# Optimization experiments

Hardware: AMD Instinct MI355X
Metric: run time of the kernel (lower is better)

The kernel has to match this reference:

```python
import jax, jax.numpy as jnp
import numpy as np

N_EMBD = 384
N_HEAD = 6
HEAD_SIZE = N_EMBD // N_HEAD  # 64
B, T, S = 128, 256, 256
EPS = 1e-5


def setup_inputs() -> dict:
    key = jax.random.key(0)
    ks = jax.random.split(key, 20)
    w = lambda k, shape: (jax.random.normal(k, shape, dtype=jnp.float32) * 0.02)
    inp = {
        'x': jax.random.normal(ks[0], (B, T, N_EMBD), dtype=jnp.float32),
        'encoder_output': jax.random.normal(ks[1], (B, S, N_EMBD), dtype=jnp.float32),
        # masked self-attention heads (stacked over heads): [H, C, D]
        'wq1': w(ks[2], (N_HEAD, N_EMBD, HEAD_SIZE)),
        'wk1': w(ks[3], (N_HEAD, N_EMBD, HEAD_SIZE)),
        'wv1': w(ks[4], (N_HEAD, N_EMBD, HEAD_SIZE)),
        'proj1_w': w(ks[5], (N_EMBD, N_EMBD)),
        'proj1_b': jnp.zeros((N_EMBD,), jnp.float32),
        # cross-attention heads
        'wq2': w(ks[6], (N_HEAD, N_EMBD, HEAD_SIZE)),
        'wk2': w(ks[7], (N_HEAD, N_EMBD, HEAD_SIZE)),
        'wv2': w(ks[8], (N_HEAD, N_EMBD, HEAD_SIZE)),
        'proj2_w': w(ks[9], (N_EMBD, N_EMBD)),
        'proj2_b': jnp.zeros((N_EMBD,), jnp.float32),
        # feed-forward
        'ffn_w1': w(ks[10], (N_EMBD, 4 * N_EMBD)),
        'ffn_b1': jnp.zeros((4 * N_EMBD,), jnp.float32),
        'ffn_w2': w(ks[11], (4 * N_EMBD, N_EMBD)),
        'ffn_b2': jnp.zeros((N_EMBD,), jnp.float32),
        # layernorms
        'ln1_g': jnp.ones((N_EMBD,), jnp.float32), 'ln1_b': jnp.zeros((N_EMBD,), jnp.float32),
        'ln2_g': jnp.ones((N_EMBD,), jnp.float32), 'ln2_b': jnp.zeros((N_EMBD,), jnp.float32),
        'ln3_g': jnp.ones((N_EMBD,), jnp.float32), 'ln3_b': jnp.zeros((N_EMBD,), jnp.float32),
    }
    return inp


def _layernorm(x, g, b):
    mu = jnp.mean(x, axis=-1, keepdims=True)
    var = jnp.mean(jnp.square(x - mu), axis=-1, keepdims=True)
    return (x - mu) * jax.lax.rsqrt(var + EPS) * g + b


def _mha(xq, xkv, wq, wk, wv, proj_w, proj_b, causal):
    # NOTE: source scales by C**-0.5 with C = n_embd (not head_size)
    scale = jnp.asarray(N_EMBD, xq.dtype) ** -0.5
    q = jnp.einsum('btc,hcd->bhtd', xq, wq)
    k = jnp.einsum('bsc,hcd->bhsd', xkv, wk)
    v = jnp.einsum('bsc,hcd->bhsd', xkv, wv)
    wei = jnp.einsum('bhtd,bhsd->bhts', q, k) * scale
    if causal:
        Tq, Tk = xq.shape[1], xkv.shape[1]
        mask = jnp.tril(jnp.ones((Tq, Tk), dtype=bool))
        wei = jnp.where(mask, wei, jnp.asarray(-jnp.inf, wei.dtype))
    p = jax.nn.softmax(wei, axis=-1)  # dropout omitted (eval mode)
    o = jnp.einsum('bhts,bhsd->bhtd', p, v)
    Bq, H, Tq, D = o.shape
    o = o.transpose(0, 2, 1, 3).reshape(Bq, Tq, H * D)  # concat heads
    return o @ proj_w + proj_b


def reference(x, encoder_output,
              wq1, wk1, wv1, proj1_w, proj1_b,
              wq2, wk2, wv2, proj2_w, proj2_b,
              ffn_w1, ffn_b1, ffn_w2, ffn_b2,
              ln1_g, ln1_b, ln2_g, ln2_b, ln3_g, ln3_b):
    # x = x + masked self-attn(ln1(x))
    x = x + _mha(_layernorm(x, ln1_g, ln1_b), _layernorm(x, ln1_g, ln1_b),
                 wq1, wk1, wv1, proj1_w, proj1_b, causal=True)
    # x = x + cross-attn(ln2(x), encoder_output)  (no mask)
    x = x + _mha(_layernorm(x, ln2_g, ln2_b), encoder_output,
                 wq2, wk2, wv2, proj2_w, proj2_b, causal=False)
    # x = x + ffwd(ln3(x))
    h = _layernorm(x, ln3_g, ln3_b)
    x = x + (jax.nn.relu(h @ ffn_w1 + ffn_b1) @ ffn_w2 + ffn_b2)
    return x
```

## Files before the change

### kernel.cpp

```cpp
#include <hip/hip_runtime.h>
#include <hip/hip_bf16.h>

#define BB 128
#define TT 256
#define CC 384
#define HH 6
#define DD 64
#define NTOK 32768

typedef __attribute__((ext_vector_type(8))) short short8;
typedef __attribute__((ext_vector_type(4))) float f32x4;

__device__ __forceinline__ unsigned short f2bf(float f) {
  union { float f; unsigned int u; } v; v.f = f;
  unsigned int r = v.u + 0x7fff + ((v.u >> 16) & 1);
  return (unsigned short)(r >> 16);
}

__device__ __forceinline__ void glds16(const void* g, void* l) {
  __builtin_amdgcn_global_load_lds((const __attribute__((address_space(1))) void*)g,
                                   (__attribute__((address_space(3))) void*)l, 16, 0, 0);
}

__device__ __forceinline__ void vm_drain() {
  asm volatile("s_waitcnt vmcnt(0)" ::: "memory");
  __builtin_amdgcn_sched_barrier(0);
}

__global__ __launch_bounds__(256) void pack_t_k(
    const float* __restrict__ wq1, const float* __restrict__ wk1, const float* __restrict__ wv1,
    const float* __restrict__ wq2, const float* __restrict__ wk2, const float* __restrict__ wv2,
    const float* __restrict__ proj1_w, const float* __restrict__ proj2_w,
    const float* __restrict__ ffn_w1, const float* __restrict__ ffn_w2,
    unsigned short* __restrict__ W) {
  __shared__ unsigned short tile[64 * 72];
  const int id = blockIdx.x;
  const int tid = threadIdx.x;
  const float* src;
  unsigned short* dst;
  int ldIn, ldOut, i0, j0;
  if (id < 216) {
    int w = id / 36, rem = id - w * 36;
    int h = rem / 6, tr = rem - h * 6;
    const float* bases[6] = {wq1, wk1, wv1, wq2, wk2, wv2};
    const int dstOff[6] = {0, 147456, 294912, 442368, 589824, 737280};
    src = bases[w] + h * 24576;
    dst = W + dstOff[w] + h * 24576;
    ldIn = 64; ldOut = 384; i0 = tr * 64; j0 = 0;
  } else if (id < 288) {
    int t = id - 216;
    int which = t / 36; t -= which * 36;
    int tr = t / 6, tc = t - tr * 6;
    src = which ? proj2_w : proj1_w;
    dst = W + (which ? 1032192 : 884736);
    ldIn = 384; ldOut = 384; i0 = tr * 64; j0 = tc * 64;
  } else if (id < 432) {
    int t = id - 288;
    int tr = t / 24, tc = t - tr * 24;
    src = ffn_w1; dst = W + 1179648;
    ldIn = 1536; ldOut = 384; i0 = tr * 64; j0 = tc * 64;
  } else {
    int t = id - 432;
    int tr = t / 6, tc = t - tr * 6;
    src = ffn_w2; dst = W + 1769472;
    ldIn = 384; ldOut = 1536; i0 = tr * 64; j0 = tc * 64;
  }
#pragma unroll
  for (int p = 0; p < 4; ++p) {
    int chunk = p * 256 + tid;
    int r = chunk >> 4, c4 = chunk & 15;
    float4 f = *(const float4*)&src[(size_t)(i0 + r) * ldIn + j0 + c4 * 4];
    tile[(c4 * 4 + 0) * 72 + r] = f2bf(f.x);
    tile[(c4 * 4 + 1) * 72 + r] = f2bf(f.y);
    tile[(c4 * 4 + 2) * 72 + r] = f2bf(f.z);
    tile[(c4 * 4 + 3) * 72 + r] = f2bf(f.w);
  }
  __syncthreads();
#pragma unroll
  for (int p = 0; p < 2; ++p) {
    int chunk = p * 256 + tid;
    int j = chunk >> 3, i8 = chunk & 7;
    *(uint4*)&dst[(size_t)(j0 + j) * ldOut + i0 + i8 * 8] = *(const uint4*)&tile[j * 72 + i8 * 8];
  }
}

__global__ __launch_bounds__(256) void ln_k(const float* __restrict__ x,
                                            unsigned short* __restrict__ out,
                                            const float* __restrict__ gamma,
                                            const float* __restrict__ beta) {
  int row = blockIdx.x * 4 + (threadIdx.x >> 6);
  int lane = threadIdx.x & 63;
  const float2* xr = (const float2*)(x + (size_t)row * CC);
  float2 v[3];
  float s = 0.f;
#pragma unroll
  for (int j = 0; j < 3; ++j) { v[j] = xr[j * 64 + lane]; s += v[j].x + v[j].y; }
#pragma unroll
  for (int m = 1; m < 64; m <<= 1) s += __shfl_xor(s, m);
  float mu = s * (1.0f / CC);
  float vs = 0.f;
#pragma unroll
  for (int j = 0; j < 3; ++j) {
    float dx = v[j].x - mu, dy = v[j].y - mu;
    vs += dx * dx + dy * dy;
  }
#pragma unroll
  for (int m = 1; m < 64; m <<= 1) vs += __shfl_xor(vs, m);
  float rs = rsqrtf(vs * (1.0f / CC) + 1e-5f);
  unsigned int* orow = (unsigned int*)(out + (size_t)row * CC);
#pragma unroll
  for (int j = 0; j < 3; ++j) {
    int cidx = j * 64 + lane;
    float2 gmm = ((const float2*)gamma)[cidx];
    float2 bt = ((const float2*)beta)[cidx];
    unsigned int lo = f2bf((v[j].x - mu) * rs * gmm.x + bt.x);
    unsigned int hi = f2bf((v[j].y - mu) * rs * gmm.y + bt.y);
    orow[cidx] = lo | (hi << 16);
  }
}

template <int EPI, bool AF32, int BM>
__global__ __launch_bounds__(256) void gemm_k(const void* __restrict__ Ap, int lda,
                                              const unsigned short* __restrict__ Bt, int ldb,
                                              void* __restrict__ Cp, int ldc,
                                              const float* __restrict__ bias,
                                              int K, int nx) {
  constexpr int MI = BM / 32;
  constexpr int APASS = BM * 8 / 256;
  __shared__ unsigned short smem[BM * 64 + 8192];
  unsigned short* sA = smem;
  unsigned short* sB = smem + BM * 64;
  const int tid = threadIdx.x;
  const int chunkg = gridDim.x >> 3;
  const int wg = blockIdx.x;
  const int lg = (wg & 7) * chunkg + (wg >> 3);
  const int bx = lg % nx, by = lg / nx;
  const int m0 = by * BM;
  const int n0 = bx * 128;
  const int wid = tid >> 6, lane = tid & 63;
  const int wr = wid >> 1, wc = wid & 1;
  const int g = lane >> 4, c = lane & 15;

  f32x4 acc[MI][4] = {};
  float biasr[4];
  if (EPI >= 1) {
#pragma unroll
    for (int ni = 0; ni < 4; ++ni) biasr[ni] = bias[n0 + wc * 64 + ni * 16 + c];
  }

  const int nt = K >> 6;
  for (int t = 0; t < nt; ++t) {
    const int k0 = t * 64;
    if constexpr (!AF32) {
#pragma unroll
      for (int p = 0; p < APASS; ++p) {
        int chunk = p * 256 + tid;
        int row = chunk >> 3, grp = chunk & 7;
        const unsigned short* Ab = (const unsigned short*)Ap;
        glds16(&Ab[(size_t)(m0 + row) * lda + k0 + ((grp ^ (row & 7)) << 3)], &sA[chunk * 8]);
      }
    } else {
#pragma unroll
      for (int p = 0; p < APASS; ++p) {
        int chunk = p * 256 + tid;
        int row = chunk >> 3, grp = chunk & 7;
        int dst = row * 64 + ((grp ^ (row & 7)) << 3);
        const float* Af = (const float*)Ap + (size_t)(m0 + row) * lda + k0 + grp * 8;
        float4 f0 = *(const float4*)Af;
        float4 f1 = *(const float4*)(Af + 4);
        union { unsigned short h[8]; uint4 u; } t2;
        t2.h[0] = f2bf(f0.x); t2.h[1] = f2bf(f0.y); t2.h[2] = f2bf(f0.z); t2.h[3] = f2bf(f0.w);
        t2.h[4] = f2bf(f1.x); t2.h[5] = f2bf(f1.y); t2.h[6] = f2bf(f1.z); t2.h[7] = f2bf(f1.w);
        *(uint4*)&sA[dst] = t2.u;
      }
    }
#pragma unroll
    for (int p = 0; p < 4; ++p) {
      int chunk = p * 256 + tid;
      int row = chunk >> 3, grp = chunk & 7;
      glds16(&Bt[(size_t)(n0 + row) * ldb + k0 + ((grp ^ (row & 7)) << 3)], &sB[chunk * 8]);
    }
    vm_drain();
    __syncthreads();
#pragma unroll
    for (int kk = 0; kk < 2; ++kk) {
      short8 a[MI], b[4];
#pragma unroll
      for (int mi = 0; mi < MI; ++mi) {
        int r = wr * (BM / 2) + mi * 16 + c;
        a[mi] = *(const short8*)&sA[r * 64 + (((kk * 4 + g) ^ (r & 7)) << 3)];
      }
#pragma unroll
      for (int ni = 0; ni < 4; ++ni) {
        int rb = wc * 64 + ni * 16 + c;
        b[ni] = *(const short8*)&sB[rb * 64 + (((kk * 4 + g) ^ (rb & 7)) << 3)];
      }
#pragma unroll
      for (int mi = 0; mi < MI; ++mi)
#pragma unroll
        for (int ni = 0; ni < 4; ++ni)
          acc[mi][ni] = __builtin_amdgcn_mfma_f32_16x16x32_bf16(a[mi], b[ni], acc[mi][ni], 0, 0, 0);
    }
    __syncthreads();
  }

#pragma unroll
  for (int mi = 0; mi < MI; ++mi)
#pragma unroll
    for (int ni = 0; ni < 4; ++ni)
#pragma unroll
      for (int i = 0; i < 4; ++i) {
        int row = wr * (BM / 2) + mi * 16 + g * 4 + i;
        int col = wc * 64 + ni * 16 + c;
        float v = acc[mi][ni][i];
        if (EPI == 1) v = fmaxf(v + biasr[ni], 0.f);
        int gsw = (col >> 3) ^ ((row >> 2) & 7);
        smem[row * 128 + gsw * 8 + (col & 7)] = f2bf(v);
      }
  __syncthreads();
#pragma unroll
  for (int it = 0; it < BM / 16; ++it) {
    int chunk = it * 256 + tid;
    int row = chunk >> 4, c16 = chunk & 15;
    int gsw = c16 ^ ((row >> 2) & 7);
    *(uint4*)&((unsigned short*)Cp)[(size_t)(m0 + row) * ldc + n0 + c16 * 8] =
        *(const uint4*)&smem[row * 128 + gsw * 8];
  }
}

__global__ __launch_bounds__(256) void ffn2_k(const unsigned short* __restrict__ h1,
                                              const unsigned short* __restrict__ W2t,
                                              float* __restrict__ out,
                                              const float* __restrict__ b2,
                                              const float* __restrict__ res) {
  __shared__ unsigned short smem[26624];
  unsigned short* sA = smem;
  unsigned short* sB = smem + 2048;
  const int tid = threadIdx.x;
  const int wg = blockIdx.x;
  const int lg = (wg & 7) * (gridDim.x >> 3) + (wg >> 3);
  const int m0 = lg * 32;
  const int w = tid >> 6, lane = tid & 63;
  const int g = lane >> 4, c = lane & 15;

  f32x4 acc[2][6] = {};
  float biasr[6];
#pragma unroll
  for (int ni = 0; ni < 6; ++ni) biasr[ni] = b2[w * 96 + ni * 16 + c];

  for (int t = 0; t < 24; ++t) {
    const int k0 = t * 64;
    {
      int row = tid >> 3, grp = tid & 7;
      glds16(&h1[(size_t)(m0 + row) * 1536 + k0 + ((grp ^ (row & 7)) << 3)], &sA[tid * 8]);
    }
#pragma unroll
    for (int p = 0; p < 12; ++p) {
      int chunk = p * 256 + tid;
      int row = chunk >> 3, grp = chunk & 7;
      glds16(&W2t[(size_t)row * 1536 + k0 + ((grp ^ (row & 7)) << 3)], &sB[chunk * 8]);
    }
    vm_drain();
    __syncthreads();
#pragma unroll
    for (int kk = 0; kk < 2; ++kk) {
      short8 a[2], b[6];
#pragma unroll
      for (int mi = 0; mi < 2; ++mi) {
        int r = mi * 16 + c;
        a[mi] = *(const short8*)&sA[r * 64 + (((kk * 4 + g) ^ (r & 7)) << 3)];
      }
#pragma unroll
      for (int ni = 0; ni < 6; ++ni) {
        int rb = w * 96 + ni * 16 + c;
        b[ni] = *(const short8*)&sB[rb * 64 + (((kk * 4 + g) ^ (rb & 7)) << 3)];
      }
#pragma unroll
      for (int mi = 0; mi < 2; ++mi)
#pragma unroll
        for (int ni = 0; ni < 6; ++ni)
          acc[mi][ni] = __builtin_amdgcn_mfma_f32_16x16x32_bf16(a[mi], b[ni], acc[mi][ni], 0, 0, 0);
    }
    __syncthreads();
  }

  float* smf = (float*)smem;
#pragma unroll
  for (int mi = 0; mi < 2; ++mi)
#pragma unroll
    for (int ni = 0; ni < 6; ++ni)
#pragma unroll
      for (int i = 0; i < 4; ++i) {
        int row = mi * 16 + g * 4 + i;
        int col = w * 96 + ni * 16 + c;
        int gg = col >> 2;
        int sg = (gg & ~7) | ((gg ^ row) & 7);
        smf[row * 388 + sg * 4 + (col & 3)] = acc[mi][ni][i] + biasr[ni];
      }
  __syncthreads();
#pragma unroll
  for (int it = 0; it < 12; ++it) {
    int chunk = it * 256 + tid;
    int row = chunk / 96, gg = chunk % 96;
    int sg = (gg & ~7) | ((gg ^ row) & 7);
    float4 v = *(const float4*)&smf[row * 388 + sg * 4];
    float4 r = *(const float4*)&res[(size_t)(m0 + row) * 384 + gg * 4];
    float4 o;
    o.x = v.x + r.x; o.y = v.y + r.y; o.z = v.z + r.z; o.w = v.w + r.w;
    *(float4*)&out[(size_t)(m0 + row) * 384 + gg * 4] = o;
  }
}

__global__ __launch_bounds__(512, 2) void gemm_ln_k(
    const unsigned short* __restrict__ Ab, const unsigned short* __restrict__ Bt,
    const float* __restrict__ bias, const float* __restrict__ res,
    float* __restrict__ xc, const float* __restrict__ gamma,
    const float* __restrict__ beta, unsigned short* __restrict__ xn) {
  __shared__ unsigned short smem[28672];
  __shared__ float part[64][8];
  unsigned short* sA = smem;
  unsigned short* sB = smem + 4096;
  const int tid = threadIdx.x;
  const int chunkg = gridDim.x >> 3;
  const int wg = blockIdx.x;
  const int lg = (wg & 7) * chunkg + (wg >> 3);
  const int m0 = lg * 64;
  const int wid = tid >> 6, lane = tid & 63;
  const int wr = wid >> 2, wcg = wid & 3;
  const int g = lane >> 4, c = lane & 15;

  f32x4 acc[2][6] = {};
  float biasr[6], gam[6], bet[6];
#pragma unroll
  for (int ni = 0; ni < 6; ++ni) {
    int col = wcg * 96 + ni * 16 + c;
    biasr[ni] = bias[col]; gam[ni] = gamma[col]; bet[ni] = beta[col];
  }

  for (int t = 0; t < 6; ++t) {
    const int k0 = t * 64;
    {
      int chunk = tid;
      int row = chunk >> 3, grp = chunk & 7;
      glds16(&Ab[(size_t)(m0 + row) * 384 + k0 + ((grp ^ (row & 7)) << 3)], &sA[chunk * 8]);
    }
#pragma unroll
    for (int p = 0; p < 6; ++p) {
      int chunk = p * 512 + tid;
      int row = chunk >> 3, grp = chunk & 7;
      glds16(&Bt[(size_t)row * 384 + k0 + ((grp ^ (row & 7)) << 3)], &sB[chunk * 8]);
    }
    vm_drain();
    __syncthreads();
#pragma unroll
    for (int kk = 0; kk < 2; ++kk) {
      short8 a[2], b[6];
#pragma unroll
      for (int mi = 0; mi < 2; ++mi) {
        int r = wr * 32 + mi * 16 + c;
        a[mi] = *(const short8*)&sA[r * 64 + (((kk * 4 + g) ^ (r & 7)) << 3)];
      }
#pragma unroll
      for (int ni = 0; ni < 6; ++ni) {
        int rb = wcg * 96 + ni * 16 + c;
        b[ni] = *(const short8*)&sB[rb * 64 + (((kk * 4 + g) ^ (rb & 7)) << 3)];
      }
#pragma unroll
      for (int mi = 0; mi < 2; ++mi)
#pragma unroll
        for (int ni = 0; ni < 6; ++ni)
          acc[mi][ni] = __builtin_amdgcn_mfma_f32_16x16x32_bf16(a[mi], b[ni], acc[mi][ni], 0, 0, 0);
    }
    __syncthreads();
  }

#pragma unroll
  for (int mi = 0; mi < 2; ++mi)
#pragma unroll
    for (int i = 0; i < 4; ++i) {
      int row = m0 + wr * 32 + mi * 16 + g * 4 + i;
#pragma unroll
      for (int ni = 0; ni < 6; ++ni)
        acc[mi][ni][i] += biasr[ni] + res[(size_t)row * 384 + wcg * 96 + ni * 16 + c];
    }

#pragma unroll
  for (int mi = 0; mi < 2; ++mi)
#pragma unroll
    for (int i = 0; i < 4; ++i) {
      float s = 0.f, q = 0.f;
#pragma unroll
      for (int ni = 0; ni < 6; ++ni) { float v = acc[mi][ni][i]; s += v; q += v * v; }
#pragma unroll
      for (int m = 1; m < 16; m <<= 1) { s += __shfl_xor(s, m); q += __shfl_xor(q, m); }
      if (c == 0) {
        int lr = wr * 32 + mi * 16 + g * 4 + i;
        part[lr][wcg] = s;
        part[lr][4 + wcg] = q;
      }
    }
  __syncthreads();
  float mu[2][4], rs[2][4];
#pragma unroll
  for (int mi = 0; mi < 2; ++mi)
#pragma unroll
    for (int i = 0; i < 4; ++i) {
      int lr = wr * 32 + mi * 16 + g * 4 + i;
      float s = part[lr][0] + part[lr][1] + part[lr][2] + part[lr][3];
      float q = part[lr][4] + part[lr][5] + part[lr][6] + part[lr][7];
      float m_ = s * (1.0f / 384.f);
      mu[mi][i] = m_;
      rs[mi][i] = rsqrtf(q * (1.0f / 384.f) - m_ * m_ + 1e-5f);
    }

  float* bf = (float*)smem;
#pragma unroll
  for (int h = 0; h < 2; ++h) {
    __syncthreads();
    if (wr == h) {
#pragma unroll
      for (int mi = 0; mi < 2; ++mi)
#pragma unroll
        for (int ni = 0; ni < 6; ++ni)
#pragma unroll
          for (int i = 0; i < 4; ++i) {
            int lr = mi * 16 + g * 4 + i;
            bf[lr * 388 + wcg * 96 + ni * 16 + c] = acc[mi][ni][i];
          }
    }
    __syncthreads();
#pragma unroll
    for (int p = 0; p < 6; ++p) {
      int chunk = p * 512 + tid;
      int row = chunk / 96, gg = chunk % 96;
      float4 v = *(const float4*)&bf[row * 388 + gg * 4];
      *(float4*)&xc[(size_t)(m0 + h * 32 + row) * 384 + gg * 4] = v;
    }
  }

  __syncthreads();
#pragma unroll
  for (int mi = 0; mi < 2; ++mi)
#pragma unroll
    for (int ni = 0; ni < 6; ++ni)
#pragma unroll
      for (int i = 0; i < 4; ++i) {
        int lr = wr * 32 + mi * 16 + g * 4 + i;
        smem[lr * 392 + wcg * 96 + ni * 16 + c] =
            f2bf((acc[mi][ni][i] - mu[mi][i]) * rs[mi][i] * gam[ni] + bet[ni]);
      }
  __syncthreads();
#pragma unroll
  for (int p = 0; p < 6; ++p) {
    int chunk = p * 512 + tid;
    int row = chunk / 48, c8 = chunk % 48;
    *(uint4*)&xn[(size_t)(m0 + row) * 384 + c8 * 8] = *(const uint4*)&smem[row * 392 + c8 * 8];
  }
}

__device__ __forceinline__ int vt_off(int d, int sgrp) {
  return d * 256 + ((((sgrp + (d >> 3)) & 31) ^ (d & 7)) << 3);
}

template <bool CAUSAL>
__global__ __launch_bounds__(512, 2) void attn_k(const unsigned short* __restrict__ QKV,
                                                 unsigned short* __restrict__ O) {
  __shared__ unsigned short Ks[256 * 64];
  __shared__ unsigned short Vt[64 * 256];
  __shared__ unsigned short Ps[8][16 * 40];
  const int bh = blockIdx.x >> 1;
  const int half = blockIdx.x & 1;
  const int b = bh / HH, hh = bh - b * HH;
  const int tid = threadIdx.x, wid = tid >> 6, lane = tid & 63;
  const int g = lane >> 4, c = lane & 15;
  const unsigned short* base = QKV + (size_t)b * TT * 1152;

#pragma unroll
  for (int t = 0; t < 4; ++t) {
    int chunk = t * 512 + tid;
    int s = chunk >> 3, grp = chunk & 7;
    *(uint4*)&Ks[s * 64 + ((grp ^ (s & 7)) << 3)] =
        *(const uint4*)&base[(size_t)s * 1152 + 384 + hh * 64 + grp * 8];
    union { unsigned short h[8]; uint4 u; } tv;
    tv.u = *(const uint4*)&base[(size_t)s * 1152 + 768 + hh * 64 + grp * 8];
#pragma unroll
    for (int j = 0; j < 8; ++j) Vt[vt_off(grp * 8 + j, s >> 3) + (s & 7)] = tv.h[j];
  }
  __syncthreads();

  const float scale = 0.05103103630798287f;
  unsigned short* Pw = &Ps[wid][0];
  const int qr0 = half * 128 + wid * 16;

  short8 aq[2];
#pragma unroll
  for (int kk = 0; kk < 2; ++kk)
    aq[kk] = *(const short8*)&QKV[(size_t)(b * TT + qr0 + c) * 1152 + hh * 64 + kk * 32 + g * 8];

  f32x4 sacc[16] = {};
#pragma unroll
  for (int sj = 0; sj < 16; ++sj) {
    if (!CAUSAL || sj * 16 <= qr0) {
      int rk = sj * 16 + c;
      f32x4 z = sacc[sj];
      z = __builtin_amdgcn_mfma_f32_16x16x32_bf16(
          aq[0], *(const short8*)&Ks[rk * 64 + ((g ^ (rk & 7)) << 3)], z, 0, 0, 0);
      z = __builtin_amdgcn_mfma_f32_16x16x32_bf16(
          aq[1], *(const short8*)&Ks[rk * 64 + (((4 + g) ^ (rk & 7)) << 3)], z, 0, 0, 0);
      sacc[sj] = z;
    }
  }

  float inv[4];
#pragma unroll
  for (int i = 0; i < 4; ++i) {
    const int qr = qr0 + g * 4 + i;
    float mx = -1e30f;
#pragma unroll
    for (int sj = 0; sj < 16; ++sj) {
      if (!CAUSAL || sj * 16 <= qr0) {
        int s = sj * 16 + c;
        float v = sacc[sj][i] * scale;
        if (CAUSAL && s > qr) v = -1e30f;
        sacc[sj][i] = v;
        mx = fmaxf(mx, v);
      }
    }
#pragma unroll
    for (int m = 1; m < 16; m <<= 1) mx = fmaxf(mx, __shfl_xor(mx, m));
    float sum = 0.f;
#pragma unroll
    for (int sj = 0; sj < 16; ++sj) {
      if (!CAUSAL || sj * 16 <= qr0) {
        float p = __expf(sacc[sj][i] - mx);
        sacc[sj][i] = p;
        sum += p;
      }
    }
#pragma unroll
    for (int m = 1; m < 16; m <<= 1) sum += __shfl_xor(sum, m);
    inv[i] = 1.0f / sum;
  }

  f32x4 oacc[4] = {};
#pragma unroll
  for (int sk = 0; sk < 8; ++sk) {
    if (!CAUSAL || sk * 32 <= qr0) {
#pragma unroll
      for (int half_sj = 0; half_sj < 2; ++half_sj) {
        int sj = sk * 2 + half_sj;
#pragma unroll
        for (int i = 0; i < 4; ++i)
          Pw[(g * 4 + i) * 40 + half_sj * 16 + c] = f2bf(sacc[sj][i]);
      }
      short8 ap = *(const short8*)&Pw[c * 40 + g * 8];
#pragma unroll
      for (int dj = 0; dj < 4; ++dj) {
        short8 bv = *(const short8*)&Vt[vt_off(dj * 16 + c, sk * 4 + g)];
        oacc[dj] = __builtin_amdgcn_mfma_f32_16x16x32_bf16(ap, bv, oacc[dj], 0, 0, 0);
      }
    }
  }

  __syncthreads();
#pragma unroll
  for (int dj = 0; dj < 4; ++dj)
#pragma unroll
    for (int i = 0; i < 4; ++i) {
      int lr = wid * 16 + g * 4 + i;
      int col = dj * 16 + c;
      int gsw = (col >> 3) ^ ((lr >> 2) & 7);
      Ks[lr * 64 + gsw * 8 + (col & 7)] = f2bf(oacc[dj][i] * inv[i]);
    }
  __syncthreads();
#pragma unroll
  for (int it = 0; it < 2; ++it) {
    int chunk = it * 512 + tid;
    int row = chunk >> 3, c8 = chunk & 7;
    int gsw = c8 ^ ((row >> 2) & 7);
    *(uint4*)&O[(size_t)(b * TT + half * 128 + row) * CC + hh * 64 + c8 * 8] =
        *(const uint4*)&Ks[row * 64 + gsw * 8];
  }
}

extern "C" void kernel_launch(void* const* d_in, const int* in_sizes, int n_in,
                              void* d_out, int out_size, void* d_ws, size_t ws_size,
                              hipStream_t stream) {
  const float* x = (const float*)d_in[0];
  const float* enc = (const float*)d_in[1];
  const float* wq1 = (const float*)d_in[2];
  const float* wk1 = (const float*)d_in[3];
  const float* wv1 = (const float*)d_in[4];
  const float* proj1_w = (const float*)d_in[5];
  const float* proj1_b = (const float*)d_in[6];
  const float* wq2 = (const float*)d_in[7];
  const float* wk2 = (const float*)d_in[8];
  const float* wv2 = (const float*)d_in[9];
  const float* proj2_w = (const float*)d_in[10];
  const float* proj2_b = (const float*)d_in[11];
  const float* ffn_w1 = (const float*)d_in[12];
  const float* ffn_b1 = (const float*)d_in[13];
  const float* ffn_w2 = (const float*)d_in[14];
  const float* ffn_b2 = (const float*)d_in[15];
  const float* ln1_g = (const float*)d_in[16];
  const float* ln1_b = (const float*)d_in[17];
  const float* ln2_g = (const float*)d_in[18];
  const float* ln2_b = (const float*)d_in[19];
  const float* ln3_g = (const float*)d_in[20];
  const float* ln3_b = (const float*)d_in[21];
  float* out = (float*)d_out;

  char* ws = (char*)d_ws;
  const size_t OFF_A = 0;
  const size_t OFF_X = 50331648;
  const size_t OFF_Q = 75497472;
  const size_t OFF_O = 150994944;
  const size_t OFF_W = 176160768;

  float* xc = (float*)(ws + OFF_A);
  unsigned short* xn = (unsigned short*)(ws + OFF_X);
  unsigned short* qkv = (unsigned short*)(ws + OFF_Q);
  unsigned short* h1 = (unsigned short*)(ws + OFF_Q);
  unsigned short* obuf = (unsigned short*)(ws + OFF_O);
  unsigned short* W = (unsigned short*)(ws + OFF_W);

  unsigned short* Wqkv1t = W + 0;
  unsigned short* Wq2t = W + 442368;
  unsigned short* Wkv2t = W + 589824;
  unsigned short* proj1t = W + 884736;
  unsigned short* proj2t = W + 1032192;
  unsigned short* W1t = W + 1179648;
  unsigned short* W2t = W + 1769472;

  pack_t_k<<<576, 256, 0, stream>>>(wq1, wk1, wv1, wq2, wk2, wv2,
                                    proj1_w, proj2_w, ffn_w1, ffn_w2, W);

  dim3 blk(256);
  ln_k<<<8192, blk, 0, stream>>>(x, xn, ln1_g, ln1_b);
  gemm_k<0, false, 128><<<2304, blk, 0, stream>>>(xn, 384, Wqkv1t, 384, qkv, 1152,
                                                  nullptr, 384, 9);
  attn_k<true><<<1536, 512, 0, stream>>>(qkv, obuf);
  gemm_ln_k<<<512, 512, 0, stream>>>(obuf, proj1t, proj1_b, x, xc, ln2_g, ln2_b, xn);
  gemm_k<0, false, 128><<<768, blk, 0, stream>>>(xn, 384, Wq2t, 384, qkv, 1152,
                                                 nullptr, 384, 3);
  gemm_k<0, true, 128><<<1536, blk, 0, stream>>>(enc, 384, Wkv2t, 384, qkv + 384, 1152,
                                                 nullptr, 384, 6);
  attn_k<false><<<1536, 512, 0, stream>>>(qkv, obuf);
  gemm_ln_k<<<512, 512, 0, stream>>>(obuf, proj2t, proj2_b, xc, xc, ln3_g, ln3_b, xn);
  gemm_k<1, false, 128><<<3072, blk, 0, stream>>>(xn, 384, W1t, 384, h1, 1536,
                                                  ffn_b1, 384, 12);
  ffn2_k<<<1024, blk, 0, stream>>>(h1, W2t, out, ffn_b2, xc);
}
```

Before: 429.1 us.

## Retile FFN2 GEMM to 64x192 blocks and remap attention blocks across XCDs

```diff
diff --git a/kernel.cpp b/kernel.cpp
--- a/kernel.cpp
+++ b/kernel.cpp
@@ -233,32 +233,37 @@
                                               float* __restrict__ out,
                                               const float* __restrict__ b2,
                                               const float* __restrict__ res) {
-  __shared__ unsigned short smem[26624];
+  __shared__ unsigned short smem[16384];
   unsigned short* sA = smem;
-  unsigned short* sB = smem + 2048;
+  unsigned short* sB = smem + 4096;
   const int tid = threadIdx.x;
   const int wg = blockIdx.x;
   const int lg = (wg & 7) * (gridDim.x >> 3) + (wg >> 3);
-  const int m0 = lg * 32;
-  const int w = tid >> 6, lane = tid & 63;
+  const int bx = lg & 1, by = lg >> 1;
+  const int m0 = by * 64;
+  const int n0 = bx * 192;
+  const int wid = tid >> 6, lane = tid & 63;
+  const int wr = wid >> 1, wc = wid & 1;
   const int g = lane >> 4, c = lane & 15;
 
   f32x4 acc[2][6] = {};
   float biasr[6];
 #pragma unroll
-  for (int ni = 0; ni < 6; ++ni) biasr[ni] = b2[w * 96 + ni * 16 + c];
+  for (int ni = 0; ni < 6; ++ni) biasr[ni] = b2[n0 + wc * 96 + ni * 16 + c];
 
   for (int t = 0; t < 24; ++t) {
     const int k0 = t * 64;
-    {
-      int row = tid >> 3, grp = tid & 7;
-      glds16(&h1[(size_t)(m0 + row) * 1536 + k0 + ((grp ^ (row & 7)) << 3)], &sA[tid * 8]);
-    }
-#pragma unroll
-    for (int p = 0; p < 12; ++p) {
+#pragma unroll
+    for (int p = 0; p < 2; ++p) {
       int chunk = p * 256 + tid;
       int row = chunk >> 3, grp = chunk & 7;
-      glds16(&W2t[(size_t)row * 1536 + k0 + ((grp ^ (row & 7)) << 3)], &sB[chunk * 8]);
+      glds16(&h1[(size_t)(m0 + row) * 1536 + k0 + ((grp ^ (row & 7)) << 3)], &sA[chunk * 8]);
+    }
+#pragma unroll
+    for (int p = 0; p < 6; ++p) {
+      int chunk = p * 256 + tid;
+      int row = chunk >> 3, grp = chunk & 7;
+      glds16(&W2t[(size_t)(n0 + row) * 1536 + k0 + ((grp ^ (row & 7)) << 3)], &sB[chunk * 8]);
     }
     vm_drain();
     __syncthreads();
@@ -267,12 +272,12 @@
       short8 a[2], b[6];
 #pragma unroll
       for (int mi = 0; mi < 2; ++mi) {
-        int r = mi * 16 + c;
+        int r = wr * 32 + mi * 16 + c;
         a[mi] = *(const short8*)&sA[r * 64 + (((kk * 4 + g) ^ (r & 7)) << 3)];
       }
 #pragma unroll
       for (int ni = 0; ni < 6; ++ni) {
-        int rb = w * 96 + ni * 16 + c;
+        int rb = wc * 96 + ni * 16 + c;
         b[ni] = *(const short8*)&sB[rb * 64 + (((kk * 4 + g) ^ (rb & 7)) << 3)];
       }
 #pragma unroll
@@ -286,28 +291,32 @@
 
   float* smf = (float*)smem;
 #pragma unroll
-  for (int mi = 0; mi < 2; ++mi)
-#pragma unroll
-    for (int ni = 0; ni < 6; ++ni)
-#pragma unroll
-      for (int i = 0; i < 4; ++i) {
-        int row = mi * 16 + g * 4 + i;
-        int col = w * 96 + ni * 16 + c;
-        int gg = col >> 2;
-        int sg = (gg & ~7) | ((gg ^ row) & 7);
-        smf[row * 388 + sg * 4 + (col & 3)] = acc[mi][ni][i] + biasr[ni];
-      }
-  __syncthreads();
-#pragma unroll
-  for (int it = 0; it < 12; ++it) {
-    int chunk = it * 256 + tid;
-    int row = chunk / 96, gg = chunk % 96;
-    int sg = (gg & ~7) | ((gg ^ row) & 7);
-    float4 v = *(const float4*)&smf[row * 388 + sg * 4];
-    float4 r = *(const float4*)&res[(size_t)(m0 + row) * 384 + gg * 4];
-    float4 o;
-    o.x = v.x + r.x; o.y = v.y + r.y; o.z = v.z + r.z; o.w = v.w + r.w;
-    *(float4*)&out[(size_t)(m0 + row) * 384 + gg * 4] = o;
+  for (int h = 0; h < 2; ++h) {
+    if (h) __syncthreads();
+    if (wr == h) {
+#pragma unroll
+      for (int mi = 0; mi < 2; ++mi)
+#pragma unroll
+        for (int ni = 0; ni < 6; ++ni)
+#pragma unroll
+          for (int i = 0; i < 4; ++i) {
+            int row = mi * 16 + g * 4 + i;
+            int col = wc * 96 + ni * 16 + c;
+            smf[row * 196 + col] = acc[mi][ni][i] + biasr[ni];
+          }
+    }
+    __syncthreads();
+#pragma unroll
+    for (int it = 0; it < 6; ++it) {
+      int chunk = it * 256 + tid;
+      int row = chunk / 48, gg = chunk % 48;
+      float4 v = *(const float4*)&smf[row * 196 + gg * 4];
+      int grow = m0 + h * 32 + row;
+      float4 r = *(const float4*)&res[(size_t)grow * 384 + n0 + gg * 4];
+      float4 o;
+      o.x = v.x + r.x; o.y = v.y + r.y; o.z = v.z + r.z; o.w = v.w + r.w;
+      *(float4*)&out[(size_t)grow * 384 + n0 + gg * 4] = o;
+    }
   }
 }
 
@@ -468,8 +477,10 @@
   __shared__ unsigned short Ks[256 * 64];
   __shared__ unsigned short Vt[64 * 256];
   __shared__ unsigned short Ps[8][16 * 40];
-  const int bh = blockIdx.x >> 1;
-  const int half = blockIdx.x & 1;
+  const int wg = blockIdx.x;
+  const int lg = (wg & 7) * (gridDim.x >> 3) + (wg >> 3);
+  const int bh = lg >> 1;
+  const int half = lg & 1;
   const int b = bh / HH, hh = bh - b * HH;
   const int tid = threadIdx.x, wid = tid >> 6, lane = tid & 63;
   const int g = lane >> 4, c = lane & 15;
```

After: 399.4 us. -6.9%, faster.
